# Optimization experiments

Hardware: AMD Instinct MI355X
Metric: run time of the kernel (lower is better)

The kernel has to match this reference:

```python
import jax, jax.numpy as jnp
import numpy as np

N = 100000
IN_C = 256
OUT_C = 64
E = 3200000


def _gcn_conv(x, src, dst, W, b, n_nodes):
    # Linear transform first (PyG GCNConv does lin then propagate)
    h = x @ W  # [N, out]
    # Symmetric normalization with self-loops already included in src/dst
    ones = jnp.ones(src.shape[0], dtype=h.dtype)
    deg = jax.ops.segment_sum(ones, dst, num_segments=n_nodes)  # in-degree incl self-loop
    dinv = jnp.where(deg > 0, jax.lax.rsqrt(deg), 0.0)
    norm = dinv[src] * dinv[dst]  # [E+N]
    msg = h[src] * norm[:, None]  # gather + scale
    out = jax.ops.segment_sum(msg, dst, num_segments=n_nodes)  # scatter-add
    return out + b


def setup_inputs() -> dict:
    key = jax.random.key(0)
    k1, k2, k3, k4, k5, k6 = jax.random.split(key, 6)
    x = jax.random.normal(k1, (N, IN_C), dtype=jnp.float32)
    edge_index = jax.random.randint(k2, (2, E), 0, N, dtype=jnp.int64)
    s = 1.0 / np.sqrt(IN_C)
    W_mu = jax.random.uniform(k3, (IN_C, OUT_C), jnp.float32, -s, s)
    b_mu = jnp.zeros((OUT_C,), jnp.float32)
    W_ls = jax.random.uniform(k4, (IN_C, OUT_C), jnp.float32, -s, s)
    b_ls = jnp.zeros((OUT_C,), jnp.float32)
    return {"x": x, "edge_index": edge_index, "W_mu": W_mu, "b_mu": b_mu, "W_ls": W_ls, "b_ls": b_ls}


def reference(x, edge_index, W_mu, b_mu, W_ls, b_ls):
    n_nodes = x.shape[0]
    loops = jnp.arange(n_nodes, dtype=edge_index.dtype)
    src = jnp.concatenate([edge_index[0], loops])  # add self-loops
    dst = jnp.concatenate([edge_index[1], loops])
    mu = _gcn_conv(x, src, dst, W_mu, b_mu, n_nodes)
    logstd = _gcn_conv(x, src, dst, W_ls, b_ls, n_nodes)
    return (mu, logstd)
```

## Files before the change

### kernel.cpp

```cpp
#include <hip/hip_runtime.h>
#include <hip/hip_bf16.h>


#define IN_C 256
#define HC   128
#define OC   64

typedef __attribute__((ext_vector_type(8))) short bf16x8;
typedef __attribute__((ext_vector_type(4))) float f32x4;

__device__ __forceinline__ short f2bf(float f) {
    union { float f; unsigned u; } v; v.f = f;
    unsigned r = v.u + 0x7fffu + ((v.u >> 16) & 1u);
    return (short)(r >> 16);
}
__device__ __forceinline__ float bf2f(short s) {
    union { float f; unsigned u; } v; v.u = ((unsigned)(unsigned short)s) << 16;
    return v.f;
}

__global__ void k_detect(const void* ei, int n_scan, long long nn, int* flag) {
    __shared__ int bad;
    if (threadIdx.x == 0) bad = 0;
    __syncthreads();
    const long long* p = (const long long*)ei;
    for (int i = threadIdx.x; i < n_scan; i += blockDim.x) {
        long long v = p[i];
        if (v < 0 || v >= nn) bad = 1;
    }
    __syncthreads();
    if (threadIdx.x == 0) *flag = bad;
}

__global__ __launch_bounds__(256) void k_zero(int* cnt, int* cursor, int n) {
    int i = blockIdx.x * 256 + threadIdx.x;
    if (i < n) { cnt[i] = 0; cursor[i] = 0; }
}

__global__ __launch_bounds__(256) void k_count(const void* ei, int* cnt, int E, const int* flag) {
    int e0 = (blockIdx.x * 256 + threadIdx.x) * 4;
    if (e0 >= E) return;
    if (e0 + 3 < E) {
        int d[4];
        if (*flag) {
            int4 v = *(const int4*)((const int*)ei + (size_t)E + e0);
            d[0] = v.x; d[1] = v.y; d[2] = v.z; d[3] = v.w;
        } else {
            const long long* p = (const long long*)ei + (size_t)E + e0;
            longlong2 a = *(const longlong2*)p;
            longlong2 b = *(const longlong2*)(p + 2);
            d[0] = (int)a.x; d[1] = (int)a.y; d[2] = (int)b.x; d[3] = (int)b.y;
        }
        #pragma unroll
        for (int u = 0; u < 4; ++u) atomicAdd(&cnt[d[u]], 1);
    } else {
        for (int e = e0; e < E; ++e) {
            int d = (*flag) ? ((const int*)ei)[(size_t)E + e]
                            : (int)((const long long*)ei)[(size_t)E + e];
            atomicAdd(&cnt[d], 1);
        }
    }
}

__global__ void k_scan(const int* __restrict__ cnt, int* __restrict__ rowptr, int n) {
    __shared__ int part[1024];
    const int tid = threadIdx.x;
    const int per = (n + 1023) >> 10;
    const int lo  = tid * per;
    const int hi  = min(lo + per, n);
    int s = 0;
    for (int i = lo; i < hi; ++i) s += cnt[i];
    part[tid] = s;
    __syncthreads();
    for (int off = 1; off < 1024; off <<= 1) {
        int v = (tid >= off) ? part[tid - off] : 0;
        __syncthreads();
        part[tid] += v;
        __syncthreads();
    }
    int run = (tid > 0) ? part[tid - 1] : 0;
    for (int i = lo; i < hi; ++i) { rowptr[i] = run; run += cnt[i]; }
    if (hi == n) rowptr[n] = run;
}

__global__ __launch_bounds__(256) void k_dinv(const int* __restrict__ cnt, float* dinv, int n) {
    int i = blockIdx.x * 256 + threadIdx.x;
    if (i < n) dinv[i] = rsqrtf((float)(cnt[i] + 1));
}

__global__ __launch_bounds__(256) void k_fill(const void* ei, const int* __restrict__ rowptr,
                                              int* cursor, int* __restrict__ esrc,
                                              int E, const int* flag) {
    int e0 = (blockIdx.x * 256 + threadIdx.x) * 4;
    if (e0 >= E) return;
    if (e0 + 3 < E) {
        int s[4], d[4];
        if (*flag) {
            int4 vs = *(const int4*)((const int*)ei + e0);
            int4 vd = *(const int4*)((const int*)ei + (size_t)E + e0);
            s[0] = vs.x; s[1] = vs.y; s[2] = vs.z; s[3] = vs.w;
            d[0] = vd.x; d[1] = vd.y; d[2] = vd.z; d[3] = vd.w;
        } else {
            const long long* ps = (const long long*)ei + e0;
            const long long* pd = (const long long*)ei + (size_t)E + e0;
            longlong2 a = *(const longlong2*)ps;
            longlong2 b = *(const longlong2*)(ps + 2);
            longlong2 c = *(const longlong2*)pd;
            longlong2 g = *(const longlong2*)(pd + 2);
            s[0] = (int)a.x; s[1] = (int)a.y; s[2] = (int)b.x; s[3] = (int)b.y;
            d[0] = (int)c.x; d[1] = (int)c.y; d[2] = (int)g.x; d[3] = (int)g.y;
        }
        #pragma unroll
        for (int u = 0; u < 4; ++u) {
            int pos = rowptr[d[u]] + atomicAdd(&cursor[d[u]], 1);
            esrc[pos] = s[u];
        }
    } else {
        for (int e = e0; e < E; ++e) {
            int s, d;
            if (*flag) {
                s = ((const int*)ei)[e]; d = ((const int*)ei)[(size_t)E + e];
            } else {
                s = (int)((const long long*)ei)[e]; d = (int)((const long long*)ei)[(size_t)E + e];
            }
            int pos = rowptr[d] + atomicAdd(&cursor[d], 1);
            esrc[pos] = s;
        }
    }
}

#define GP 40
__global__ __launch_bounds__(256) void k_gemm(const float* __restrict__ x,
                                              const float* __restrict__ Wmu,
                                              const float* __restrict__ Wls,
                                              float* __restrict__ hout, int nrows) {
    __shared__ short Ah[128][GP], Al[128][GP];
    __shared__ short Bh[128][GP], Bl[128][GP];
    const int tid  = threadIdx.x;
    const int wid  = tid >> 6;
    const int lane = tid & 63;
    const int l15  = lane & 15;
    const int k0   = (lane >> 4) * 8;
    const size_t rowbase = (size_t)blockIdx.x * 128;

    f32x4 acc[2][8];
    #pragma unroll
    for (int rt = 0; rt < 2; ++rt)
        #pragma unroll
        for (int ct = 0; ct < 8; ++ct) acc[rt][ct] = (f32x4){0.f, 0.f, 0.f, 0.f};

    for (int kc = 0; kc < IN_C; kc += 32) {
        __syncthreads();
        #pragma unroll
        for (int it = 0; it < 4; ++it) {
            int q = tid + 256 * it;
            int r = q >> 3, f = q & 7;
            size_t gr = rowbase + r;
            float4 v = make_float4(0.f, 0.f, 0.f, 0.f);
            if (gr < (size_t)nrows)
                v = *(const float4*)(x + gr * IN_C + kc + f * 4);
            short h0 = f2bf(v.x), h1 = f2bf(v.y), h2 = f2bf(v.z), h3 = f2bf(v.w);
            short l0 = f2bf(v.x - bf2f(h0)), l1 = f2bf(v.y - bf2f(h1));
            short l2 = f2bf(v.z - bf2f(h2)), l3 = f2bf(v.w - bf2f(h3));
            *(ushort4*)&Ah[r][f * 4] = make_ushort4((unsigned short)h0, (unsigned short)h1,
                                                    (unsigned short)h2, (unsigned short)h3);
            *(ushort4*)&Al[r][f * 4] = make_ushort4((unsigned short)l0, (unsigned short)l1,
                                                    (unsigned short)l2, (unsigned short)l3);
        }
        #pragma unroll
        for (int it = 0; it < 2; ++it) {
            int q = tid + 256 * it;
            int c = q >> 2, g = q & 3;
            const float* wc = (c < OC) ? (Wmu + c) : (Wls + (c - OC));
            short hb[8], lb[8];
            #pragma unroll
            for (int j = 0; j < 8; ++j) {
                float v = wc[(size_t)(kc + g * 8 + j) * OC];
                short h = f2bf(v);
                hb[j] = h;
                lb[j] = f2bf(v - bf2f(h));
            }
            *(bf16x8*)&Bh[c][g * 8] = *(bf16x8*)hb;
            *(bf16x8*)&Bl[c][g * 8] = *(bf16x8*)lb;
        }
        __syncthreads();

        bf16x8 ah[2], al[2];
        #pragma unroll
        for (int rt = 0; rt < 2; ++rt) {
            int r = rt * 64 + wid * 16 + l15;
            ah[rt] = *(bf16x8*)&Ah[r][k0];
            al[rt] = *(bf16x8*)&Al[r][k0];
        }
        #pragma unroll
        for (int ct = 0; ct < 8; ++ct) {
            bf16x8 bh = *(bf16x8*)&Bh[ct * 16 + l15][k0];
            bf16x8 bl = *(bf16x8*)&Bl[ct * 16 + l15][k0];
            #pragma unroll
            for (int rt = 0; rt < 2; ++rt) {
                acc[rt][ct] = __builtin_amdgcn_mfma_f32_16x16x32_bf16(al[rt], bh, acc[rt][ct], 0, 0, 0);
                acc[rt][ct] = __builtin_amdgcn_mfma_f32_16x16x32_bf16(ah[rt], bl, acc[rt][ct], 0, 0, 0);
                acc[rt][ct] = __builtin_amdgcn_mfma_f32_16x16x32_bf16(ah[rt], bh, acc[rt][ct], 0, 0, 0);
            }
        }
    }

    const int orow = (lane >> 4) * 4;
    #pragma unroll
    for (int rt = 0; rt < 2; ++rt)
        #pragma unroll
        for (int ct = 0; ct < 8; ++ct)
            #pragma unroll
            for (int rg = 0; rg < 4; ++rg) {
                size_t grow = rowbase + rt * 64 + wid * 16 + orow + rg;
                if (grow < (size_t)nrows)
                    hout[grow * HC + ct * 16 + l15] = acc[rt][ct][rg];
            }
}

__global__ __launch_bounds__(256) void k_out(const float* __restrict__ h,
                                             const int* __restrict__ rowptr,
                                             const int* __restrict__ esrc,
                                             const float* __restrict__ dinv,
                                             const float* __restrict__ bmu,
                                             const float* __restrict__ bls,
                                             float* __restrict__ out_mu,
                                             float* __restrict__ out_ls, int n) {
    int node = blockIdx.x * 4 + (threadIdx.x >> 6);
    if (node >= n) return;
    int lane = threadIdx.x & 63;
    const float2* __restrict__ h2 = (const float2*)h;

    float di = dinv[node];
    float2 self = h2[(size_t)node * 64 + lane];
    float w  = di * di;
    float ax = self.x * w, ay = self.y * w;

    int k   = rowptr[node];
    int end = rowptr[node + 1];

    for (; k + 7 < end; k += 8) {
        int   s[8];
        float nm[8];
        float2 v[8];
        #pragma unroll
        for (int u = 0; u < 8; ++u) s[u] = esrc[k + u];
        #pragma unroll
        for (int u = 0; u < 8; ++u) nm[u] = dinv[s[u]] * di;
        #pragma unroll
        for (int u = 0; u < 8; ++u) v[u] = h2[(size_t)s[u] * 64 + lane];
        #pragma unroll
        for (int u = 0; u < 8; ++u) { ax += v[u].x * nm[u]; ay += v[u].y * nm[u]; }
    }
    for (; k < end; ++k) {
        int s0 = esrc[k];
        float n0 = dinv[s0] * di;
        float2 v0 = h2[(size_t)s0 * 64 + lane];
        ax += v0.x * n0;
        ay += v0.y * n0;
    }

    if (lane < 32) {
        float2 b = ((const float2*)bmu)[lane];
        ((float2*)out_mu)[(size_t)node * 32 + lane] = make_float2(ax + b.x, ay + b.y);
    } else {
        float2 b = ((const float2*)bls)[lane - 32];
        ((float2*)out_ls)[(size_t)node * 32 + (lane - 32)] = make_float2(ax + b.x, ay + b.y);
    }
}

extern "C" void kernel_launch(void* const* d_in, const int* in_sizes, int n_in,
                              void* d_out, int out_size, void* d_ws, size_t ws_size,
                              hipStream_t stream) {
    const float* x   = (const float*)d_in[0];
    const void*  ei  = d_in[1];
    const float* Wmu = (const float*)d_in[2];
    const float* bmu = (const float*)d_in[3];
    const float* Wls = (const float*)d_in[4];
    const float* bls = (const float*)d_in[5];

    const int N = in_sizes[0] / IN_C;
    const int E = in_sizes[1] / 2;

    float* out_mu = (float*)d_out;
    float* out_ls = (float*)d_out + (size_t)N * OC;

    char* w = (char*)d_ws;
    auto align256 = [](size_t v) { return (v + 255) & ~(size_t)255; };
    int*   flag   = (int*)w;                  size_t off = 256;
    int*   cnt    = (int*)(w + off);          off += align256((size_t)N * 4);
    int*   cursor = (int*)(w + off);          off += align256((size_t)N * 4);
    float* dinv   = (float*)(w + off);        off += align256((size_t)N * 4);
    int*   rowptr = (int*)(w + off);          off += align256((size_t)(N + 1) * 4);
    int*   esrc   = (int*)(w + off);          off += align256((size_t)E * 4);
    float* h      = (float*)(w + off);        off += align256((size_t)N * HC * 4);

    int n_scan = E < 4096 ? E : 4096;
    hipLaunchKernelGGL(k_detect, dim3(1), dim3(256), 0, stream, ei, n_scan, (long long)N, flag);

    int gN = (N + 255) / 256;
    hipLaunchKernelGGL(k_zero, dim3(gN), dim3(256), 0, stream, cnt, cursor, N);

    int gE4 = (E + 1023) / 1024;
    hipLaunchKernelGGL(k_count, dim3(gE4), dim3(256), 0, stream, ei, cnt, E, flag);

    hipLaunchKernelGGL(k_scan, dim3(1), dim3(1024), 0, stream, cnt, rowptr, N);
    hipLaunchKernelGGL(k_dinv, dim3(gN), dim3(256), 0, stream, cnt, dinv, N);
    hipLaunchKernelGGL(k_fill, dim3(gE4), dim3(256), 0, stream, ei, rowptr, cursor, esrc, E, flag);

    int gG = (N + 127) / 128;
    hipLaunchKernelGGL(k_gemm, dim3(gG), dim3(256), 0, stream, x, Wmu, Wls, h, N);

    int gO = (N + 3) / 4;
    hipLaunchKernelGGL(k_out, dim3(gO), dim3(256), 0, stream, h, rowptr, esrc, dinv, bmu, bls, out_mu, out_ls, N);
}
```

Before: 908.6 us.

## Parallelize CSR prefix scan across blocks and split edges between wave halves

Replaces the single-block 1024-thread scan with a three-stage multi-block scan that also computes dinv and zeroes the cursor array, which removes the separate dinv kernel and the cursor zeroing. The aggregation kernel now has each half-wave process alternate edges with float4 loads covering all 128 features, then combines the halves with a cross-lane shuffle. The intent is to remove the serial single-block scan bottleneck and to keep more independent gathers in flight per wave. The cost is extra kernel launches and a shuffle reduction step in each wave.

```diff
diff --git a/kernel.cpp b/kernel.cpp
--- a/kernel.cpp
+++ b/kernel.cpp
@@ -5,6 +5,7 @@
 #define IN_C 256
 #define HC   128
 #define OC   64
+#define SCHUNK 4096
 
 typedef __attribute__((ext_vector_type(8))) short bf16x8;
 typedef __attribute__((ext_vector_type(4))) float f32x4;
@@ -32,9 +33,9 @@
     if (threadIdx.x == 0) *flag = bad;
 }
 
-__global__ __launch_bounds__(256) void k_zero(int* cnt, int* cursor, int n) {
+__global__ __launch_bounds__(256) void k_zero(int* cnt, int n) {
     int i = blockIdx.x * 256 + threadIdx.x;
-    if (i < n) { cnt[i] = 0; cursor[i] = 0; }
+    if (i < n) cnt[i] = 0;
 }
 
 __global__ __launch_bounds__(256) void k_count(const void* ei, int* cnt, int E, const int* flag) {
@@ -62,30 +63,81 @@
     }
 }
 
-__global__ void k_scan(const int* __restrict__ cnt, int* __restrict__ rowptr, int n) {
-    __shared__ int part[1024];
+__global__ __launch_bounds__(256) void k_scan1(const int* __restrict__ cnt, int* __restrict__ bsum, int n) {
+    __shared__ int red[256];
     const int tid = threadIdx.x;
-    const int per = (n + 1023) >> 10;
-    const int lo  = tid * per;
-    const int hi  = min(lo + per, n);
+    int lo = blockIdx.x * SCHUNK + tid * 16;
     int s = 0;
-    for (int i = lo; i < hi; ++i) s += cnt[i];
+    if (lo < n) {
+        int hi = min(lo + 16, n);
+        if (hi == lo + 16) {
+            #pragma unroll
+            for (int q = 0; q < 4; ++q) {
+                int4 v = *(const int4*)(cnt + lo + q * 4);
+                s += v.x + v.y + v.z + v.w;
+            }
+        } else {
+            for (int i = lo; i < hi; ++i) s += cnt[i];
+        }
+    }
+    red[tid] = s;
+    __syncthreads();
+    for (int off = 128; off > 0; off >>= 1) {
+        if (tid < off) red[tid] += red[tid + off];
+        __syncthreads();
+    }
+    if (tid == 0) bsum[blockIdx.x] = red[0];
+}
+
+__global__ void k_scan2(const int* __restrict__ bsum, int* __restrict__ bbase, int nb) {
+    if (threadIdx.x == 0) {
+        int run = 0;
+        for (int b = 0; b < nb; ++b) { bbase[b] = run; run += bsum[b]; }
+    }
+}
+
+__global__ __launch_bounds__(256) void k_scan3(const int* __restrict__ cnt,
+                                               const int* __restrict__ bbase,
+                                               int* __restrict__ rowptr,
+                                               float* __restrict__ dinv,
+                                               int* __restrict__ cursor, int n) {
+    __shared__ int part[256];
+    const int tid = threadIdx.x;
+    int lo = blockIdx.x * SCHUNK + tid * 16;
+    int loc[16];
+    int s = 0, cntv = 0;
+    if (lo < n) {
+        cntv = min(lo + 16, n) - lo;
+        if (cntv == 16) {
+            #pragma unroll
+            for (int q = 0; q < 4; ++q) {
+                int4 v = *(const int4*)(cnt + lo + q * 4);
+                loc[q * 4 + 0] = v.x; loc[q * 4 + 1] = v.y;
+                loc[q * 4 + 2] = v.z; loc[q * 4 + 3] = v.w;
+            }
+        } else {
+            for (int u = 0; u < cntv; ++u) loc[u] = cnt[lo + u];
+        }
+        for (int u = 0; u < cntv; ++u) s += loc[u];
+    }
     part[tid] = s;
     __syncthreads();
-    for (int off = 1; off < 1024; off <<= 1) {
+    for (int off = 1; off < 256; off <<= 1) {
         int v = (tid >= off) ? part[tid - off] : 0;
         __syncthreads();
         part[tid] += v;
         __syncthreads();
     }
-    int run = (tid > 0) ? part[tid - 1] : 0;
-    for (int i = lo; i < hi; ++i) { rowptr[i] = run; run += cnt[i]; }
-    if (hi == n) rowptr[n] = run;
-}
-
-__global__ __launch_bounds__(256) void k_dinv(const int* __restrict__ cnt, float* dinv, int n) {
-    int i = blockIdx.x * 256 + threadIdx.x;
-    if (i < n) dinv[i] = rsqrtf((float)(cnt[i] + 1));
+    if (lo < n) {
+        int run = bbase[blockIdx.x] + (tid ? part[tid - 1] : 0);
+        for (int u = 0; u < cntv; ++u) {
+            rowptr[lo + u] = run;
+            dinv[lo + u]   = rsqrtf((float)(loc[u] + 1));
+            cursor[lo + u] = 0;
+            run += loc[u];
+        }
+        if (lo + cntv == n) rowptr[n] = run;
+    }
 }
 
 __global__ __launch_bounds__(256) void k_fill(const void* ei, const int* __restrict__ rowptr,
@@ -228,44 +280,58 @@
                                              float* __restrict__ out_ls, int n) {
     int node = blockIdx.x * 4 + (threadIdx.x >> 6);
     if (node >= n) return;
-    int lane = threadIdx.x & 63;
-    const float2* __restrict__ h2 = (const float2*)h;
+    const int lane = threadIdx.x & 63;
+    const int half = lane >> 5;
+    const int j    = lane & 31;
+    const float4* __restrict__ h4 = (const float4*)h;
 
     float di = dinv[node];
-    float2 self = h2[(size_t)node * 64 + lane];
-    float w  = di * di;
-    float ax = self.x * w, ay = self.y * w;
-
-    int k   = rowptr[node];
+    float4 acc = make_float4(0.f, 0.f, 0.f, 0.f);
+    if (half == 0) {
+        float w = di * di;
+        float4 self = h4[(size_t)node * 32 + j];
+        acc = make_float4(self.x * w, self.y * w, self.z * w, self.w * w);
+    }
+
+    int k   = rowptr[node] + half;
     int end = rowptr[node + 1];
 
-    for (; k + 7 < end; k += 8) {
-        int   s[8];
-        float nm[8];
-        float2 v[8];
-        #pragma unroll
-        for (int u = 0; u < 8; ++u) s[u] = esrc[k + u];
-        #pragma unroll
-        for (int u = 0; u < 8; ++u) nm[u] = dinv[s[u]] * di;
-        #pragma unroll
-        for (int u = 0; u < 8; ++u) v[u] = h2[(size_t)s[u] * 64 + lane];
-        #pragma unroll
-        for (int u = 0; u < 8; ++u) { ax += v[u].x * nm[u]; ay += v[u].y * nm[u]; }
-    }
-    for (; k < end; ++k) {
+    for (; k + 6 < end; k += 8) {
+        int s0 = esrc[k], s1 = esrc[k + 2], s2 = esrc[k + 4], s3 = esrc[k + 6];
+        float n0 = dinv[s0] * di, n1 = dinv[s1] * di, n2 = dinv[s2] * di, n3 = dinv[s3] * di;
+        float4 v0 = h4[(size_t)s0 * 32 + j];
+        float4 v1 = h4[(size_t)s1 * 32 + j];
+        float4 v2 = h4[(size_t)s2 * 32 + j];
+        float4 v3 = h4[(size_t)s3 * 32 + j];
+        acc.x += v0.x * n0 + v1.x * n1 + v2.x * n2 + v3.x * n3;
+        acc.y += v0.y * n0 + v1.y * n1 + v2.y * n2 + v3.y * n3;
+        acc.z += v0.z * n0 + v1.z * n1 + v2.z * n2 + v3.z * n3;
+        acc.w += v0.w * n0 + v1.w * n1 + v2.w * n2 + v3.w * n3;
+    }
+    for (; k < end; k += 2) {
         int s0 = esrc[k];
         float n0 = dinv[s0] * di;
-        float2 v0 = h2[(size_t)s0 * 64 + lane];
-        ax += v0.x * n0;
-        ay += v0.y * n0;
-    }
+        float4 v0 = h4[(size_t)s0 * 32 + j];
+        acc.x += v0.x * n0; acc.y += v0.y * n0;
+        acc.z += v0.z * n0; acc.w += v0.w * n0;
+    }
+
+    acc.x += __shfl_xor(acc.x, 32);
+    acc.y += __shfl_xor(acc.y, 32);
+    acc.z += __shfl_xor(acc.z, 32);
+    acc.w += __shfl_xor(acc.w, 32);
 
     if (lane < 32) {
-        float2 b = ((const float2*)bmu)[lane];
-        ((float2*)out_mu)[(size_t)node * 32 + lane] = make_float2(ax + b.x, ay + b.y);
-    } else {
-        float2 b = ((const float2*)bls)[lane - 32];
-        ((float2*)out_ls)[(size_t)node * 32 + (lane - 32)] = make_float2(ax + b.x, ay + b.y);
+        if (j < 16) {
+            float4 b = ((const float4*)bmu)[j];
+            ((float4*)out_mu)[(size_t)node * 16 + j] =
+                make_float4(acc.x + b.x, acc.y + b.y, acc.z + b.z, acc.w + b.w);
+        } else {
+            int jj = j - 16;
+            float4 b = ((const float4*)bls)[jj];
+            ((float4*)out_ls)[(size_t)node * 16 + jj] =
+                make_float4(acc.x + b.x, acc.y + b.y, acc.z + b.z, acc.w + b.w);
+        }
     }
 }
 
@@ -288,6 +354,8 @@
     char* w = (char*)d_ws;
     auto align256 = [](size_t v) { return (v + 255) & ~(size_t)255; };
     int*   flag   = (int*)w;                  size_t off = 256;
+    int*   bsum   = (int*)(w + off);          off += 256;
+    int*   bbase  = (int*)(w + off);          off += 256;
     int*   cnt    = (int*)(w + off);          off += align256((size_t)N * 4);
     int*   cursor = (int*)(w + off);          off += align256((size_t)N * 4);
     float* dinv   = (float*)(w + off);        off += align256((size_t)N * 4);
@@ -299,13 +367,16 @@
     hipLaunchKernelGGL(k_detect, dim3(1), dim3(256), 0, stream, ei, n_scan, (long long)N, flag);
 
     int gN = (N + 255) / 256;
-    hipLaunchKernelGGL(k_zero, dim3(gN), dim3(256), 0, stream, cnt, cursor, N);
+    hipLaunchKernelGGL(k_zero, dim3(gN), dim3(256), 0, stream, cnt, N);
 
     int gE4 = (E + 1023) / 1024;
     hipLaunchKernelGGL(k_count, dim3(gE4), dim3(256), 0, stream, ei, cnt, E, flag);
 
-    hipLaunchKernelGGL(k_scan, dim3(1), dim3(1024), 0, stream, cnt, rowptr, N);
-    hipLaunchKernelGGL(k_dinv, dim3(gN), dim3(256), 0, stream, cnt, dinv, N);
+    int nb = (N + SCHUNK - 1) / SCHUNK;
+    hipLaunchKernelGGL(k_scan1, dim3(nb), dim3(256), 0, stream, cnt, bsum, N);
+    hipLaunchKernelGGL(k_scan2, dim3(1), dim3(64), 0, stream, bsum, bbase, nb);
+    hipLaunchKernelGGL(k_scan3, dim3(nb), dim3(256), 0, stream, cnt, bbase, rowptr, dinv, cursor, N);
+
     hipLaunchKernelGGL(k_fill, dim3(gE4), dim3(256), 0, stream, ei, rowptr, cursor, esrc, E, flag);
 
     int gG = (N + 127) / 128;
```

Measured after the change: 758.8 us. 1.2x faster.
